# Optimization experiments

Measured on AMD Instinct MI355X. Metric: run time of the kernel, lower is better.

The kernel has to match this reference:

```python
import jax, jax.numpy as jnp
import numpy as np

FP8_MAX = 448.0  # max finite value of float8_e4m3fn


def quantize_tensorwise(x):
    """Tensorwise fp8 quantization: returns fp8 tensor and inverse scale."""
    amax = jnp.max(jnp.abs(x))
    inv_scale = jnp.maximum(amax, jnp.asarray(1e-12, x.dtype)) / FP8_MAX
    q = (x / inv_scale).astype(jnp.float8_e4m3fn)
    return q, inv_scale


def setup_inputs() -> dict:
    key = jax.random.key(0)
    k1, k2, k3 = jax.random.split(key, 3)
    x = jax.random.normal(k1, (4, 1024, 4096), dtype=jnp.float32)
    weight = jax.random.normal(k2, (4096, 4096), dtype=jnp.float32) * 0.02
    bias = jax.random.normal(k3, (4096,), dtype=jnp.float32)
    return {"x": x, "weight": weight, "bias": bias}


def reference(x, weight, bias):
    out_shape = (*x.shape[:-1], weight.shape[0])
    xm = x.reshape(-1, x.shape[-1])                    # [M, K]
    fp8_x, x_inv_scale = quantize_tensorwise(xm)       # fp8 input + tensorwise scale
    fp8_wt, w_inv_scale = quantize_tensorwise(weight.T)  # weight.t() quantized, [K, N]
    # fp8 GEMM with inline dequant: (fp8_x @ fp8_w.T) * sx * sw + bias
    acc = jnp.matmul(fp8_x.astype(jnp.float32), fp8_wt.astype(jnp.float32))
    out = acc * (x_inv_scale * w_inv_scale) + bias.astype(jnp.float32)
    return out.reshape(out_shape).astype(x.dtype)
```

## Files before the change

### kernel.cpp

```cpp
#include <hip/hip_runtime.h>
#include <hip/hip_bf16.h>
#include <stdint.h>

static constexpr int M = 4096, N = 4096, K = 4096;
static constexpr float FP8_MAX = 448.0f;

using f32x16 = __attribute__((ext_vector_type(16))) float;
using i32x4  = __attribute__((ext_vector_type(4))) int;
using i32x8  = __attribute__((ext_vector_type(8))) int;

static constexpr size_t AQ_OFF   = 0;
static constexpr size_t BQ_OFF   = (size_t)M * K;
static constexpr size_t AMAX_OFF = BQ_OFF + (size_t)N * K;

__global__ __launch_bounds__(256) void amax_kernel(const float* __restrict__ x,
                                                   const float* __restrict__ w,
                                                   float* __restrict__ amax,
                                                   int n4_per_tensor,
                                                   int blocks_per_tensor) {
    const int tensor = blockIdx.x / blocks_per_tensor;
    const int blk    = blockIdx.x % blocks_per_tensor;
    const float4* src = (const float4*)(tensor == 0 ? x : w);

    float m = 0.0f;
    for (int i = blk * blockDim.x + threadIdx.x; i < n4_per_tensor;
         i += blocks_per_tensor * blockDim.x) {
        float4 v = src[i];
        m = fmaxf(m, fmaxf(fmaxf(fabsf(v.x), fabsf(v.y)),
                           fmaxf(fabsf(v.z), fabsf(v.w))));
    }
    #pragma unroll
    for (int off = 32; off >= 1; off >>= 1)
        m = fmaxf(m, __shfl_xor(m, off, 64));

    __shared__ float sm[4];
    const int lane = threadIdx.x & 63, wid = threadIdx.x >> 6;
    if (lane == 0) sm[wid] = m;
    __syncthreads();
    if (threadIdx.x == 0) {
        m = fmaxf(fmaxf(sm[0], sm[1]), fmaxf(sm[2], sm[3]));
        atomicMax((unsigned int*)&amax[tensor], __float_as_uint(m));
    }
}

__global__ __launch_bounds__(256) void quant_kernel(const float* __restrict__ x,
                                                    const float* __restrict__ w,
                                                    unsigned char* __restrict__ aq,
                                                    unsigned char* __restrict__ bq,
                                                    const float* __restrict__ amax,
                                                    int n4_per_tensor) {
    int gid = blockIdx.x * blockDim.x + threadIdx.x;
    const int tensor = (gid >= n4_per_tensor) ? 1 : 0;
    const int i = tensor ? gid - n4_per_tensor : gid;

    const float inv = fmaxf(amax[tensor], 1e-12f) / FP8_MAX;
    const float4* src = (const float4*)(tensor == 0 ? x : w);

    float4 v = src[i];
    float q0 = v.x / inv, q1 = v.y / inv, q2 = v.z / inv, q3 = v.w / inv;
    int packed = __builtin_amdgcn_cvt_pk_fp8_f32(q0, q1, 0, false);
    packed     = __builtin_amdgcn_cvt_pk_fp8_f32(q2, q3, packed, true);

    if (tensor == 0) {
        ((int*)aq)[i] = packed;
    } else {
        const int n  = i >> 10;
        const int k0 = (i & 1023) * 4;
        const int blk = (n >> 5) * (K / 64) + (k0 >> 6);
        const int ln  = (n & 31) + 32 * ((k0 >> 5) & 1);
        ((int*)bq)[blk * 512 + ln * 8 + ((k0 >> 2) & 7)] = packed;
    }
}

static constexpr int BM = 128, BN = 256, BK = 64, DEPTH = 4, NT = K / BK;

__device__ __forceinline__ void gld_lds16(const void* g, void* l) {
    __builtin_amdgcn_global_load_lds(
        (const __attribute__((address_space(1))) void*)g,
        (__attribute__((address_space(3))) void*)l, 16, 0, 0);
}

struct BPair { i32x8 b0, b1; };

__global__ __launch_bounds__(512, 4) void gemm_kernel(const unsigned char* __restrict__ Aq,
                                                      const unsigned char* __restrict__ Bq,
                                                      const float* __restrict__ amax,
                                                      const float* __restrict__ bias,
                                                      float* __restrict__ out) {
    __shared__ unsigned char lds[DEPTH][BM * BK];

    const int tid  = threadIdx.x;
    const int lane = tid & 63;
    const int w    = tid >> 6;
    const int wr   = w >> 2, wc = w & 3;

    const int bid = blockIdx.x;
    const int swz = (bid & 7) * 64 + (bid >> 3);
    const int brow = (swz >> 4) * BM;
    const int bcol = (swz & 15) * BN;

    const float sx = fmaxf(amax[0], 1e-12f) / FP8_MAX;
    const float sw = fmaxf(amax[1], 1e-12f) / FP8_MAX;
    const float scale = sx * sw;

    const int row0  = tid >> 2;
    const int chk   = ((tid & 3) ^ ((row0 >> 1) & 3)) * 16;
    const unsigned char* Abase = Aq + (size_t)brow * K;

    const int frow = lane & 31;
    const int swzr = (frow >> 1) & 3;
    const int c0   = (lane >> 5) * 2;
    const int off0 = ((c0 ^ swzr) << 4);
    const int off1 = (((c0 + 1) ^ swzr) << 4);

    const unsigned char* Bf0 =
        Bq + (size_t)((bcol >> 5) + wc * 2 + 0) * (K / 64) * 2048 + (size_t)lane * 32;
    const unsigned char* Bf1 =
        Bq + (size_t)((bcol >> 5) + wc * 2 + 1) * (K / 64) * 2048 + (size_t)lane * 32;

    f32x16 acc[2][2] = {};

#define STAGE_A(t, d)                                                          \
    gld_lds16(Abase + (size_t)row0 * K + (size_t)(t) * BK + chk,               \
              &lds[d][(tid >> 6) * 1024])

#define GLOAD_B(t, BR)                                                         \
    do {                                                                       \
        const size_t _o = (size_t)(t) * 2048;                                  \
        BR.b0 = *(const i32x8*)(Bf0 + _o);                                     \
        BR.b1 = *(const i32x8*)(Bf1 + _o);                                     \
    } while (0)

#define ITER(t, rs, ss, BCUR, BNXT)                                            \
    do {                                                                       \
        asm volatile("s_waitcnt vmcnt(1)" ::: "memory");                       \
        __builtin_amdgcn_s_barrier();                                          \
        __builtin_amdgcn_sched_barrier(0);                                     \
        GLOAD_B(((t) + 1 < NT) ? (t) + 1 : NT - 1, BNXT);                      \
        STAGE_A(((t) + 3 < NT) ? (t) + 3 : NT - 1, ss);                        \
        i32x8 _a0, _a1;                                                        \
        {                                                                      \
            const unsigned char* _p = &lds[rs][(wr * 64 + frow) * BK];         \
            i32x4 _lo = *(const i32x4*)(_p + off0);                            \
            i32x4 _hi = *(const i32x4*)(_p + off1);                            \
            _a0 = __builtin_shufflevector(_lo, _hi, 0, 1, 2, 3, 4, 5, 6, 7);   \
        }                                                                      \
        {                                                                      \
            const unsigned char* _p = &lds[rs][(wr * 64 + 32 + frow) * BK];    \
            i32x4 _lo = *(const i32x4*)(_p + off0);                            \
            i32x4 _hi = *(const i32x4*)(_p + off1);                            \
            _a1 = __builtin_shufflevector(_lo, _hi, 0, 1, 2, 3, 4, 5, 6, 7);   \
        }                                                                      \
        __builtin_amdgcn_s_setprio(1);                                         \
        acc[0][0] = __builtin_amdgcn_mfma_scale_f32_32x32x64_f8f6f4(           \
            _a0, BCUR.b0, acc[0][0], 0, 0, 0, 0x7F, 0, 0x7F);                  \
        acc[0][1] = __builtin_amdgcn_mfma_scale_f32_32x32x64_f8f6f4(           \
            _a0, BCUR.b1, acc[0][1], 0, 0, 0, 0x7F, 0, 0x7F);                  \
        acc[1][0] = __builtin_amdgcn_mfma_scale_f32_32x32x64_f8f6f4(           \
            _a1, BCUR.b0, acc[1][0], 0, 0, 0, 0x7F, 0, 0x7F);                  \
        acc[1][1] = __builtin_amdgcn_mfma_scale_f32_32x32x64_f8f6f4(           \
            _a1, BCUR.b1, acc[1][1], 0, 0, 0, 0x7F, 0, 0x7F);                  \
        __builtin_amdgcn_s_setprio(0);                                         \
        asm volatile("s_waitcnt lgkmcnt(0)" ::: "memory");                     \
        __builtin_amdgcn_sched_barrier(0);                                     \
    } while (0)

    BPair bP, bQ;

    STAGE_A(0, 0);
    STAGE_A(1, 1);
    STAGE_A(2, 2);
    GLOAD_B(0, bP);
    asm volatile("s_waitcnt vmcnt(0)" ::: "memory");
    __builtin_amdgcn_s_barrier();
    __builtin_amdgcn_sched_barrier(0);

    for (int t = 0; t < NT; t += 4) {
        ITER(t + 0, 0, 3, bP, bQ);
        ITER(t + 1, 1, 0, bQ, bP);
        ITER(t + 2, 2, 1, bP, bQ);
        ITER(t + 3, 3, 2, bQ, bP);
    }
#undef ITER
#undef GLOAD_B
#undef STAGE_A

    #pragma unroll
    for (int mt = 0; mt < 2; ++mt) {
        const int rbase = brow + wr * 64 + mt * 32 + 4 * (lane >> 5);
        #pragma unroll
        for (int nt2 = 0; nt2 < 2; ++nt2) {
            const int col = bcol + wc * 64 + nt2 * 32 + (lane & 31);
            const float b = bias[col];
            #pragma unroll
            for (int reg = 0; reg < 16; ++reg) {
                const int row = rbase + (reg & 3) + 8 * (reg >> 2);
                out[(size_t)row * N + col] = acc[mt][nt2][reg] * scale + b;
            }
        }
    }
}

extern "C" void kernel_launch(void* const* d_in, const int* in_sizes, int n_in,
                              void* d_out, int out_size, void* d_ws, size_t ws_size,
                              hipStream_t stream) {
    const float* x    = (const float*)d_in[0];
    const float* w    = (const float*)d_in[1];
    const float* bias = (const float*)d_in[2];
    float* out = (float*)d_out;

    unsigned char* aq = (unsigned char*)d_ws + AQ_OFF;
    unsigned char* bq = (unsigned char*)d_ws + BQ_OFF;
    float* amax = (float*)((unsigned char*)d_ws + AMAX_OFF);

    const int n4 = (M * K) / 4;

    hipMemsetAsync(amax, 0, 2 * sizeof(float), stream);

    const int blocks_per_tensor = 512;
    amax_kernel<<<2 * blocks_per_tensor, 256, 0, stream>>>(x, w, amax, n4, blocks_per_tensor);

    const int quant_blocks = (2 * n4) / 256;
    quant_kernel<<<quant_blocks, 256, 0, stream>>>(x, w, aq, bq, amax, n4);

    gemm_kernel<<<512, 512, 0, stream>>>(aq, bq, amax, bias, out);
}
```

Measured before the change: 143.0 us.

## Restructure GEMM into single-wave 128x64 blocks without workgroup barriers

Replaces the 8-wave 128x256 GEMM workgroup with 2048 single-wave workgroups, each computing a 128x64 tile. Each wave stages the whole A tile into LDS and accumulates 4x2 MFMA tiles. This removes the s_barrier and lgkmcnt synchronisation, relying on vmcnt counting alone. In exchange each B column block is loaded by many more workgroups, so global and L2 traffic goes up. LDS use per wave rises and fewer waves share one LDS tile.

```diff
diff --git a/kernel.cpp b/kernel.cpp
--- a/kernel.cpp
+++ b/kernel.cpp
@@ -72,7 +72,7 @@
     }
 }
 
-static constexpr int BM = 128, BN = 256, BK = 64, DEPTH = 4, NT = K / BK;
+static constexpr int BK = 64, DEPTH = 4, NT = K / BK;
 
 __device__ __forceinline__ void gld_lds16(const void* g, void* l) {
     __builtin_amdgcn_global_load_lds(
@@ -82,30 +82,27 @@
 
 struct BPair { i32x8 b0, b1; };
 
-__global__ __launch_bounds__(512, 4) void gemm_kernel(const unsigned char* __restrict__ Aq,
-                                                      const unsigned char* __restrict__ Bq,
-                                                      const float* __restrict__ amax,
-                                                      const float* __restrict__ bias,
-                                                      float* __restrict__ out) {
-    __shared__ unsigned char lds[DEPTH][BM * BK];
-
-    const int tid  = threadIdx.x;
-    const int lane = tid & 63;
-    const int w    = tid >> 6;
-    const int wr   = w >> 2, wc = w & 3;
+__global__ __launch_bounds__(64, 2) void gemm_kernel(const unsigned char* __restrict__ Aq,
+                                                     const unsigned char* __restrict__ Bq,
+                                                     const float* __restrict__ amax,
+                                                     const float* __restrict__ bias,
+                                                     float* __restrict__ out) {
+    __shared__ unsigned char lds[DEPTH][128 * BK];
+
+    const int lane = threadIdx.x & 63;
 
     const int bid = blockIdx.x;
-    const int swz = (bid & 7) * 64 + (bid >> 3);
-    const int brow = (swz >> 4) * BM;
-    const int bcol = (swz & 15) * BN;
+    const int swz = (bid & 7) * 256 + (bid >> 3);
+    const int brow = (swz & 31) * 128;
+    const int bcol = (swz >> 5) * 64;
 
     const float sx = fmaxf(amax[0], 1e-12f) / FP8_MAX;
     const float sw = fmaxf(amax[1], 1e-12f) / FP8_MAX;
     const float scale = sx * sw;
 
-    const int row0  = tid >> 2;
-    const int chk   = ((tid & 3) ^ ((row0 >> 1) & 3)) * 16;
-    const unsigned char* Abase = Aq + (size_t)brow * K;
+    const int r4  = lane >> 2;
+    const int chk = ((lane & 3) ^ ((r4 >> 1) & 3)) * 16;
+    const unsigned char* Abase = Aq + (size_t)brow * K + (size_t)r4 * K + chk;
 
     const int frow = lane & 31;
     const int swzr = (frow >> 1) & 3;
@@ -114,15 +111,19 @@
     const int off1 = (((c0 + 1) ^ swzr) << 4);
 
     const unsigned char* Bf0 =
-        Bq + (size_t)((bcol >> 5) + wc * 2 + 0) * (K / 64) * 2048 + (size_t)lane * 32;
+        Bq + (size_t)((bcol >> 5) + 0) * (K / 64) * 2048 + (size_t)lane * 32;
     const unsigned char* Bf1 =
-        Bq + (size_t)((bcol >> 5) + wc * 2 + 1) * (K / 64) * 2048 + (size_t)lane * 32;
-
-    f32x16 acc[2][2] = {};
+        Bq + (size_t)((bcol >> 5) + 1) * (K / 64) * 2048 + (size_t)lane * 32;
+
+    f32x16 acc[4][2] = {};
 
 #define STAGE_A(t, d)                                                          \
-    gld_lds16(Abase + (size_t)row0 * K + (size_t)(t) * BK + chk,               \
-              &lds[d][(tid >> 6) * 1024])
+    do {                                                                       \
+        _Pragma("unroll")                                                      \
+        for (int _o = 0; _o < 8; ++_o)                                         \
+            gld_lds16(Abase + (size_t)(_o * 16) * K + (size_t)(t) * BK,        \
+                      &lds[d][_o * 1024]);                                     \
+    } while (0)
 
 #define GLOAD_B(t, BR)                                                         \
     do {                                                                       \
@@ -133,47 +134,34 @@
 
 #define ITER(t, rs, ss, BCUR, BNXT)                                            \
     do {                                                                       \
-        asm volatile("s_waitcnt vmcnt(1)" ::: "memory");                       \
-        __builtin_amdgcn_s_barrier();                                          \
-        __builtin_amdgcn_sched_barrier(0);                                     \
+        asm volatile("s_waitcnt vmcnt(8)" ::: "memory");                       \
         GLOAD_B(((t) + 1 < NT) ? (t) + 1 : NT - 1, BNXT);                      \
         STAGE_A(((t) + 3 < NT) ? (t) + 3 : NT - 1, ss);                        \
-        i32x8 _a0, _a1;                                                        \
-        {                                                                      \
-            const unsigned char* _p = &lds[rs][(wr * 64 + frow) * BK];         \
+        i32x8 _aF[4];                                                          \
+        _Pragma("unroll")                                                      \
+        for (int _mt = 0; _mt < 4; ++_mt) {                                    \
+            const unsigned char* _p = &lds[rs][(_mt * 32 + frow) * BK];        \
             i32x4 _lo = *(const i32x4*)(_p + off0);                            \
             i32x4 _hi = *(const i32x4*)(_p + off1);                            \
-            _a0 = __builtin_shufflevector(_lo, _hi, 0, 1, 2, 3, 4, 5, 6, 7);   \
-        }                                                                      \
-        {                                                                      \
-            const unsigned char* _p = &lds[rs][(wr * 64 + 32 + frow) * BK];    \
-            i32x4 _lo = *(const i32x4*)(_p + off0);                            \
-            i32x4 _hi = *(const i32x4*)(_p + off1);                            \
-            _a1 = __builtin_shufflevector(_lo, _hi, 0, 1, 2, 3, 4, 5, 6, 7);   \
+            _aF[_mt] = __builtin_shufflevector(_lo, _hi, 0, 1, 2, 3, 4, 5, 6, 7); \
         }                                                                      \
         __builtin_amdgcn_s_setprio(1);                                         \
-        acc[0][0] = __builtin_amdgcn_mfma_scale_f32_32x32x64_f8f6f4(           \
-            _a0, BCUR.b0, acc[0][0], 0, 0, 0, 0x7F, 0, 0x7F);                  \
-        acc[0][1] = __builtin_amdgcn_mfma_scale_f32_32x32x64_f8f6f4(           \
-            _a0, BCUR.b1, acc[0][1], 0, 0, 0, 0x7F, 0, 0x7F);                  \
-        acc[1][0] = __builtin_amdgcn_mfma_scale_f32_32x32x64_f8f6f4(           \
-            _a1, BCUR.b0, acc[1][0], 0, 0, 0, 0x7F, 0, 0x7F);                  \
-        acc[1][1] = __builtin_amdgcn_mfma_scale_f32_32x32x64_f8f6f4(           \
-            _a1, BCUR.b1, acc[1][1], 0, 0, 0, 0x7F, 0, 0x7F);                  \
+        _Pragma("unroll")                                                      \
+        for (int _mt = 0; _mt < 4; ++_mt) {                                    \
+            acc[_mt][0] = __builtin_amdgcn_mfma_scale_f32_32x32x64_f8f6f4(     \
+                _aF[_mt], BCUR.b0, acc[_mt][0], 0, 0, 0, 0x7F, 0, 0x7F);       \
+            acc[_mt][1] = __builtin_amdgcn_mfma_scale_f32_32x32x64_f8f6f4(     \
+                _aF[_mt], BCUR.b1, acc[_mt][1], 0, 0, 0, 0x7F, 0, 0x7F);       \
+        }                                                                      \
         __builtin_amdgcn_s_setprio(0);                                         \
-        asm volatile("s_waitcnt lgkmcnt(0)" ::: "memory");                     \
-        __builtin_amdgcn_sched_barrier(0);                                     \
     } while (0)
 
     BPair bP, bQ;
 
     STAGE_A(0, 0);
+    GLOAD_B(0, bP);
     STAGE_A(1, 1);
     STAGE_A(2, 2);
-    GLOAD_B(0, bP);
-    asm volatile("s_waitcnt vmcnt(0)" ::: "memory");
-    __builtin_amdgcn_s_barrier();
-    __builtin_amdgcn_sched_barrier(0);
 
     for (int t = 0; t < NT; t += 4) {
         ITER(t + 0, 0, 3, bP, bQ);
@@ -186,11 +174,11 @@
 #undef STAGE_A
 
     #pragma unroll
-    for (int mt = 0; mt < 2; ++mt) {
-        const int rbase = brow + wr * 64 + mt * 32 + 4 * (lane >> 5);
+    for (int mt = 0; mt < 4; ++mt) {
+        const int rbase = brow + mt * 32 + 4 * (lane >> 5);
         #pragma unroll
         for (int nt2 = 0; nt2 < 2; ++nt2) {
-            const int col = bcol + wc * 64 + nt2 * 32 + (lane & 31);
+            const int col = bcol + nt2 * 32 + (lane & 31);
             const float b = bias[col];
             #pragma unroll
             for (int reg = 0; reg < 16; ++reg) {
@@ -223,5 +211,5 @@
     const int quant_blocks = (2 * n4) / 256;
     quant_kernel<<<quant_blocks, 256, 0, stream>>>(x, w, aq, bq, amax, n4);
 
-    gemm_kernel<<<512, 512, 0, stream>>>(aq, bq, amax, bias, out);
-}
+    gemm_kernel<<<2048, 64, 0, stream>>>(aq, bq, amax, bias, out);
+}
```

Result: slower. 168.8 us (+18.1%).

## Pre-swizzle A into fragment layout and load both operands directly from global

Applied to the files above, without the earlier changes.

The quantize kernel now writes the activation matrix in the same MFMA fragment-blocked layout already used for the weights. This lets the GEMM drop LDS staging of A and the barriers it needed: every wave loads its A and B fragments straight from global memory into registers, double-buffered two tiles ahead. The aim is to remove LDS traffic and block-wide synchronisation. In exchange, A fragments are no longer shared between the waves of a block through LDS, so global/L2 read traffic rises, and register pressure grows, with the occupancy hint lowered to 2.

```diff
diff --git a/kernel.cpp b/kernel.cpp
--- a/kernel.cpp
+++ b/kernel.cpp
@@ -55,40 +55,29 @@
 
     const float inv = fmaxf(amax[tensor], 1e-12f) / FP8_MAX;
     const float4* src = (const float4*)(tensor == 0 ? x : w);
+    int* dst = (int*)(tensor == 0 ? aq : bq);
 
     float4 v = src[i];
     float q0 = v.x / inv, q1 = v.y / inv, q2 = v.z / inv, q3 = v.w / inv;
     int packed = __builtin_amdgcn_cvt_pk_fp8_f32(q0, q1, 0, false);
     packed     = __builtin_amdgcn_cvt_pk_fp8_f32(q2, q3, packed, true);
 
-    if (tensor == 0) {
-        ((int*)aq)[i] = packed;
-    } else {
-        const int n  = i >> 10;
-        const int k0 = (i & 1023) * 4;
-        const int blk = (n >> 5) * (K / 64) + (k0 >> 6);
-        const int ln  = (n & 31) + 32 * ((k0 >> 5) & 1);
-        ((int*)bq)[blk * 512 + ln * 8 + ((k0 >> 2) & 7)] = packed;
-    }
+    const int r  = i >> 10;
+    const int k0 = (i & 1023) * 4;
+    const int blk = (r >> 5) * (K / 64) + (k0 >> 6);
+    const int ln  = (r & 31) + 32 * ((k0 >> 5) & 1);
+    dst[blk * 512 + ln * 8 + ((k0 >> 2) & 7)] = packed;
 }
 
-static constexpr int BM = 128, BN = 256, BK = 64, DEPTH = 4, NT = K / BK;
+static constexpr int BK = 64, NT = K / BK;
 
-__device__ __forceinline__ void gld_lds16(const void* g, void* l) {
-    __builtin_amdgcn_global_load_lds(
-        (const __attribute__((address_space(1))) void*)g,
-        (__attribute__((address_space(3))) void*)l, 16, 0, 0);
-}
+struct FragSet { i32x8 a0, a1, b0, b1; };
 
-struct BPair { i32x8 b0, b1; };
-
-__global__ __launch_bounds__(512, 4) void gemm_kernel(const unsigned char* __restrict__ Aq,
+__global__ __launch_bounds__(512, 2) void gemm_kernel(const unsigned char* __restrict__ Aq,
                                                       const unsigned char* __restrict__ Bq,
                                                       const float* __restrict__ amax,
                                                       const float* __restrict__ bias,
                                                       float* __restrict__ out) {
-    __shared__ unsigned char lds[DEPTH][BM * BK];
-
     const int tid  = threadIdx.x;
     const int lane = tid & 63;
     const int w    = tid >> 6;
@@ -96,94 +85,56 @@
 
     const int bid = blockIdx.x;
     const int swz = (bid & 7) * 64 + (bid >> 3);
-    const int brow = (swz >> 4) * BM;
-    const int bcol = (swz & 15) * BN;
+    const int brow = (swz >> 4) * 128;
+    const int bcol = (swz & 15) * 256;
 
     const float sx = fmaxf(amax[0], 1e-12f) / FP8_MAX;
     const float sw = fmaxf(amax[1], 1e-12f) / FP8_MAX;
     const float scale = sx * sw;
 
-    const int row0  = tid >> 2;
-    const int chk   = ((tid & 3) ^ ((row0 >> 1) & 3)) * 16;
-    const unsigned char* Abase = Aq + (size_t)brow * K;
-
-    const int frow = lane & 31;
-    const int swzr = (frow >> 1) & 3;
-    const int c0   = (lane >> 5) * 2;
-    const int off0 = ((c0 ^ swzr) << 4);
-    const int off1 = (((c0 + 1) ^ swzr) << 4);
-
-    const unsigned char* Bf0 =
-        Bq + (size_t)((bcol >> 5) + wc * 2 + 0) * (K / 64) * 2048 + (size_t)lane * 32;
-    const unsigned char* Bf1 =
-        Bq + (size_t)((bcol >> 5) + wc * 2 + 1) * (K / 64) * 2048 + (size_t)lane * 32;
+    const size_t KB = (size_t)(K / 64) * 2048;
+    const unsigned char* Af0 = Aq + (size_t)((brow >> 5) + wr * 2 + 0) * KB + (size_t)lane * 32;
+    const unsigned char* Af1 = Aq + (size_t)((brow >> 5) + wr * 2 + 1) * KB + (size_t)lane * 32;
+    const unsigned char* Bf0 = Bq + (size_t)((bcol >> 5) + wc * 2 + 0) * KB + (size_t)lane * 32;
+    const unsigned char* Bf1 = Bq + (size_t)((bcol >> 5) + wc * 2 + 1) * KB + (size_t)lane * 32;
 
     f32x16 acc[2][2] = {};
 
-#define STAGE_A(t, d)                                                          \
-    gld_lds16(Abase + (size_t)row0 * K + (size_t)(t) * BK + chk,               \
-              &lds[d][(tid >> 6) * 1024])
-
-#define GLOAD_B(t, BR)                                                         \
+#define LOADF(t, S)                                                            \
     do {                                                                       \
         const size_t _o = (size_t)(t) * 2048;                                  \
-        BR.b0 = *(const i32x8*)(Bf0 + _o);                                     \
-        BR.b1 = *(const i32x8*)(Bf1 + _o);                                     \
+        S.a0 = *(const i32x8*)(Af0 + _o);                                      \
+        S.a1 = *(const i32x8*)(Af1 + _o);                                      \
+        S.b0 = *(const i32x8*)(Bf0 + _o);                                      \
+        S.b1 = *(const i32x8*)(Bf1 + _o);                                      \
     } while (0)
 
-#define ITER(t, rs, ss, BCUR, BNXT)                                            \
+#define MX(a, b, c) \
+    __builtin_amdgcn_mfma_scale_f32_32x32x64_f8f6f4((a), (b), (c), 0, 0, 0, 0x7F, 0, 0x7F)
+
+#define ITER(t, S)                                                             \
     do {                                                                       \
-        asm volatile("s_waitcnt vmcnt(1)" ::: "memory");                       \
-        __builtin_amdgcn_s_barrier();                                          \
-        __builtin_amdgcn_sched_barrier(0);                                     \
-        GLOAD_B(((t) + 1 < NT) ? (t) + 1 : NT - 1, BNXT);                      \
-        STAGE_A(((t) + 3 < NT) ? (t) + 3 : NT - 1, ss);                        \
-        i32x8 _a0, _a1;                                                        \
-        {                                                                      \
-            const unsigned char* _p = &lds[rs][(wr * 64 + frow) * BK];         \
-            i32x4 _lo = *(const i32x4*)(_p + off0);                            \
-            i32x4 _hi = *(const i32x4*)(_p + off1);                            \
-            _a0 = __builtin_shufflevector(_lo, _hi, 0, 1, 2, 3, 4, 5, 6, 7);   \
-        }                                                                      \
-        {                                                                      \
-            const unsigned char* _p = &lds[rs][(wr * 64 + 32 + frow) * BK];    \
-            i32x4 _lo = *(const i32x4*)(_p + off0);                            \
-            i32x4 _hi = *(const i32x4*)(_p + off1);                            \
-            _a1 = __builtin_shufflevector(_lo, _hi, 0, 1, 2, 3, 4, 5, 6, 7);   \
-        }                                                                      \
         __builtin_amdgcn_s_setprio(1);                                         \
-        acc[0][0] = __builtin_amdgcn_mfma_scale_f32_32x32x64_f8f6f4(           \
-            _a0, BCUR.b0, acc[0][0], 0, 0, 0, 0x7F, 0, 0x7F);                  \
-        acc[0][1] = __builtin_amdgcn_mfma_scale_f32_32x32x64_f8f6f4(           \
-            _a0, BCUR.b1, acc[0][1], 0, 0, 0, 0x7F, 0, 0x7F);                  \
-        acc[1][0] = __builtin_amdgcn_mfma_scale_f32_32x32x64_f8f6f4(           \
-            _a1, BCUR.b0, acc[1][0], 0, 0, 0, 0x7F, 0, 0x7F);                  \
-        acc[1][1] = __builtin_amdgcn_mfma_scale_f32_32x32x64_f8f6f4(           \
-            _a1, BCUR.b1, acc[1][1], 0, 0, 0, 0x7F, 0, 0x7F);                  \
+        acc[0][0] = MX(S.a0, S.b0, acc[0][0]);                                 \
+        acc[0][1] = MX(S.a0, S.b1, acc[0][1]);                                 \
+        acc[1][0] = MX(S.a1, S.b0, acc[1][0]);                                 \
+        acc[1][1] = MX(S.a1, S.b1, acc[1][1]);                                 \
         __builtin_amdgcn_s_setprio(0);                                         \
-        asm volatile("s_waitcnt lgkmcnt(0)" ::: "memory");                     \
+        LOADF(((t) + 2 < NT) ? (t) + 2 : NT - 1, S);                           \
         __builtin_amdgcn_sched_barrier(0);                                     \
     } while (0)
 
-    BPair bP, bQ;
+    FragSet s0, s1;
+    LOADF(0, s0);
+    LOADF(1, s1);
 
-    STAGE_A(0, 0);
-    STAGE_A(1, 1);
-    STAGE_A(2, 2);
-    GLOAD_B(0, bP);
-    asm volatile("s_waitcnt vmcnt(0)" ::: "memory");
-    __builtin_amdgcn_s_barrier();
-    __builtin_amdgcn_sched_barrier(0);
-
-    for (int t = 0; t < NT; t += 4) {
-        ITER(t + 0, 0, 3, bP, bQ);
-        ITER(t + 1, 1, 0, bQ, bP);
-        ITER(t + 2, 2, 1, bP, bQ);
-        ITER(t + 3, 3, 2, bQ, bP);
+    for (int t = 0; t < NT; t += 2) {
+        ITER(t + 0, s0);
+        ITER(t + 1, s1);
     }
 #undef ITER
-#undef GLOAD_B
-#undef STAGE_A
+#undef MX
+#undef LOADF
 
     #pragma unroll
     for (int mt = 0; mt < 2; ++mt) {
```

New measurement: 164.2 us. 14.8% more time.
